# Kernel tuning notes

Hardware: AMD Instinct MI355X
Metric: run time of the kernel (lower is better)

The kernel has to match this reference:

```python
import jax, jax.numpy as jnp
import numpy as np

D_MODEL = 1024
NHEAD = 16
D_K = D_MODEL // NHEAD
NEG_INF = -1e30


def setup_inputs() -> dict:
    key = jax.random.key(0)
    ks = jax.random.split(key, 5)
    seq, batch = 2048, 4
    scale_in = 1.0 / np.sqrt(D_MODEL)
    return {
        "x": jax.random.normal(ks[0], (seq, batch, D_MODEL), dtype=jnp.float32),
        # torch nn.Linear stores weight as (out_features, in_features)
        "w_qkv": jax.random.normal(ks[1], (3 * D_MODEL, D_MODEL), dtype=jnp.float32) * scale_in,
        "b_qkv": jax.random.normal(ks[2], (3 * D_MODEL,), dtype=jnp.float32) * 0.01,
        "w_out": jax.random.normal(ks[3], (D_MODEL, D_MODEL), dtype=jnp.float32) * scale_in,
        "b_out": jax.random.normal(ks[4], (D_MODEL,), dtype=jnp.float32) * 0.01,
        "causal": 1,
    }


def reference(x, w_qkv, b_qkv, w_out, b_out, causal):
    seq, batch, d_model = x.shape
    # fused QKV projection: (seq, batch, 3*d_model)
    qkv = jnp.einsum("sbd,ed->sbe", x, w_qkv) + b_qkv
    q, k, v = jnp.split(qkv, 3, axis=-1)

    def to_heads(t):
        # (seq, batch, d_model) -> (batch*nhead, seq, d_k)
        return t.reshape(seq, batch * NHEAD, D_K).transpose(1, 0, 2)

    q, k, v = to_heads(q), to_heads(k), to_heads(v)
    # full O(seq^2) score tensor, matching the manual implementation
    scores = jnp.einsum("hqd,hkd->hqk", q, k) / (D_K ** 0.5)
    if causal:  # causal is a static Python int, safe under jit as constant
        mask = jnp.triu(jnp.ones((seq, seq), dtype=bool), k=1)
        scores = jnp.where(mask[None, :, :], NEG_INF, scores)
    attn = jax.nn.softmax(scores, axis=-1)
    out = jnp.einsum("hqk,hkd->hqd", attn, v)  # (batch*nhead, seq, d_k)
    out = out.transpose(1, 0, 2).reshape(seq, batch, d_model)
    return jnp.einsum("sbd,ed->sbe", out, w_out) + b_out
```

## Files before the change

### kernel.cpp

```cpp
#include <hip/hip_runtime.h>

typedef __attribute__((ext_vector_type(8))) short short8;
typedef __attribute__((ext_vector_type(4))) float floatx4;
typedef __attribute__((ext_vector_type(16))) float floatx16;
typedef __attribute__((ext_vector_type(4))) unsigned short ushort4v;

__device__ __forceinline__ unsigned short f2bf(float f) {
  unsigned int u = __float_as_uint(f);
  u += 0x7FFFu + ((u >> 16) & 1u);
  return (unsigned short)(u >> 16);
}

__device__ __forceinline__ unsigned int cvt_pk_bf16(float lo, float hi) {
  unsigned int r;
  asm("v_cvt_pk_bf16_f32 %0, %1, %2" : "=v"(r) : "v"(lo), "v"(hi));
  return r;
}

__device__ __forceinline__ void async_copy16(const void* g, void* l) {
  __builtin_amdgcn_global_load_lds(
      (const __attribute__((address_space(1))) unsigned int*)g,
      (__attribute__((address_space(3))) unsigned int*)l, 16, 0, 0);
}

__device__ __forceinline__ float fexp2(float x) {
#if __has_builtin(__builtin_amdgcn_exp2f)
  return __builtin_amdgcn_exp2f(x);
#else
  return exp2f(x);
#endif
}

__global__ __launch_bounds__(256) void cvt_all(const float* __restrict__ x,
                                               const float* __restrict__ wq,
                                               const float* __restrict__ wo,
                                               unsigned short* __restrict__ Xb,
                                               unsigned short* __restrict__ Wqb,
                                               unsigned short* __restrict__ Wob) {
  int i = blockIdx.x * blockDim.x + threadIdx.x;
  const float* src;
  unsigned short* dst;
  int off;
  if (i < 2097152) { src = x;  dst = Xb;  off = i; }
  else if (i < 2883584) { src = wq; dst = Wqb; off = i - 2097152; }
  else { src = wo; dst = Wob; off = i - 2883584; }
  float4 v = reinterpret_cast<const float4*>(src)[off];
  ushort4v o;
  o[0] = f2bf(v.x); o[1] = f2bf(v.y); o[2] = f2bf(v.z); o[3] = f2bf(v.w);
  reinterpret_cast<ushort4v*>(dst)[off] = o;
}

template <int MODE, int NX>
__global__ __launch_bounds__(256, 4) void gemm_nt(const unsigned short* __restrict__ A,
                                                  const unsigned short* __restrict__ B,
                                                  const float* __restrict__ bias,
                                                  void* __restrict__ C,
                                                  int M, int N, int K) {
  __shared__ __align__(16) unsigned short lds[2][128 * 64];
  unsigned short* lA = lds[0];
  unsigned short* lB = lds[1];
  unsigned short* lflat = &lds[0][0];
  const int tid = threadIdx.x;
  const int lane = tid & 63, wave = tid >> 6;
  const int lr = lane & 15, lh = lane >> 4;
  const int chunk = gridDim.x >> 3;
  const int g2 = (blockIdx.x & 7) * chunk + (blockIdx.x >> 3);
  const int m0 = (g2 / NX) * 128, n0 = (g2 % NX) * 128;
  const int wm = (wave >> 1) * 64, wn = (wave & 1) * 64;
  floatx4 acc[4][4] = {};

  for (int k0 = 0; k0 < K; k0 += 64) {
    __syncthreads();
#pragma unroll
    for (int c0 = 0; c0 < 1024; c0 += 256) {
      int L = c0 + tid;
      int r = L >> 3;
      int c = (L & 7) ^ (r & 7);
      async_copy16(A + (size_t)(m0 + r) * K + k0 + c * 8, &lA[(size_t)(c0 + wave * 64) * 8]);
      async_copy16(B + (size_t)(n0 + r) * K + k0 + c * 8, &lB[(size_t)(c0 + wave * 64) * 8]);
    }
    __syncthreads();
#pragma unroll
    for (int kk = 0; kk < 2; ++kk) {
      short8 af[4], bfr[4];
#pragma unroll
      for (int mf = 0; mf < 4; ++mf)
        af[mf] = *(const short8*)&lA[(wm + mf * 16 + lr) * 64 + (((kk * 4 + lh) ^ (lr & 7)) * 8)];
#pragma unroll
      for (int nf = 0; nf < 4; ++nf)
        bfr[nf] = *(const short8*)&lB[(wn + nf * 16 + lr) * 64 + (((kk * 4 + lh) ^ (lr & 7)) * 8)];
#pragma unroll
      for (int mf = 0; mf < 4; ++mf)
#pragma unroll
        for (int nf = 0; nf < 4; ++nf)
          acc[mf][nf] = __builtin_amdgcn_mfma_f32_16x16x32_bf16(af[mf], bfr[nf], acc[mf][nf], 0, 0, 0);
    }
  }

  if (MODE == 1 && (n0 >> 10) == 2) {
    __syncthreads();
#pragma unroll
    for (int mf = 0; mf < 4; ++mf) {
      int sl = (wm >> 2) + mf * 4 + lh;
#pragma unroll
      for (int nf = 0; nf < 4; ++nf) {
        int cl = wn + nf * 16 + lr;
        int hh = cl >> 6, dd = cl & 63;
        int sx = sl ^ ((dd & 3) << 3);
#pragma unroll
        for (int r = 0; r < 4; ++r) {
          float v = acc[mf][nf][r] + bias[n0 + cl];
          lflat[((r * 2 + hh) * 64 + dd) * 32 + sx] = f2bf(v);
        }
      }
    }
    __syncthreads();
    const int hbase = (n0 & 1023) >> 6;
    const int s0g = m0 >> 2;
    unsigned short* V = (unsigned short*)C + (size_t)2 * 64 * 2048 * 64;
#pragma unroll
    for (int k = 0; k < 8; ++k) {
      int f = tid + k * 256;
      int p = f >> 2, q = f & 3;
      int b = p >> 7, hh = (p >> 6) & 1, dd = p & 63;
      int g = b * 16 + hbase + hh;
      int sc = (q ^ (dd & 3)) * 8;
      short8 vv = *(const short8*)&lflat[p * 32 + q * 8];
      *(short8*)&V[((size_t)g * 64 + dd) * 2048 + s0g + sc] = vv;
    }
  } else {
#pragma unroll
    for (int mf = 0; mf < 4; ++mf)
#pragma unroll
      for (int nf = 0; nf < 4; ++nf)
#pragma unroll
        for (int r = 0; r < 4; ++r) {
          int row = m0 + wm + mf * 16 + lh * 4 + r;
          int col = n0 + wn + nf * 16 + lr;
          float v = acc[mf][nf][r] + bias[col];
          if (MODE == 0) {
            ((float*)C)[(size_t)row * N + col] = v;
          } else {
            int part = col >> 10, wi = col & 1023;
            int h = wi >> 6, dd = wi & 63;
            int s = row >> 2, b = row & 3;
            int gg = b * 16 + h;
            size_t base = (size_t)part * (64u * 2048u * 64u);
            if (part == 0) v *= 0.18033688011112042f;
            ((unsigned short*)C)[base + ((size_t)gg * 2048 + s) * 64 + dd] = f2bf(v);
          }
        }
  }
}

__global__ __launch_bounds__(256) void attn_fwd(const unsigned short* __restrict__ Qb,
                                                const unsigned short* __restrict__ Kb,
                                                const unsigned short* __restrict__ Vt,
                                                unsigned short* __restrict__ Att,
                                                const int* __restrict__ causal_p) {
  __shared__ __align__(16) unsigned short smem[16384];
  const int tid = threadIdx.x;
  const int lane = tid & 63, w = tid >> 6;
  const int l31 = lane & 31, hi = lane >> 5;
  const int bid = blockIdx.x;
  const int jj = (bid >> 3) & 3;
  const int mm = (bid >> 5) & 3;
  const int kk2 = (bid >> 8) & 3;
  const int g = (bid & 7) + 8 * ((bid >> 7) & 1) + 16 * mm;
  const int qt = (kk2 == 0) ? (15 - jj) : (kk2 == 1) ? jj : (kk2 == 2) ? (11 - jj) : (4 + jj);
  const int q0 = qt * 128;
  const int causal = causal_p[0];
  const size_t headOff = (size_t)g * 2048 * 64;
  const size_t vtHead = (size_t)g * 64 * 2048;
  const int q0w = q0 + w * 32;
  const int qg = q0w + l31;

  short8 qf[4];
#pragma unroll
  for (int c = 0; c < 4; ++c)
    qf[c] = *(const short8*)&Qb[headOff + (size_t)qg * 64 + c * 16 + hi * 8];

  floatx16 oacc[2] = {};
  float mrow = -1e30f, lrow = 0.f;

  const int nt = causal ? (q0 + 128) / 64 : 2048 / 64;
  const int qmax_w = q0w + 31;

  auto stageK = [&](int buf, int kv0) {
#pragma unroll
    for (int c0 = 0; c0 < 512; c0 += 256) {
      int L = c0 + tid;
      int kvr = L >> 3;
      int c = (tid & 7) ^ (kvr & 7);
      async_copy16(Kb + headOff + (size_t)(kv0 + kvr) * 64 + c * 8,
                   &smem[(size_t)buf * 4096 + (size_t)(c0 + w * 64) * 8]);
    }
  };
  auto stageV = [&](int buf, int kv0) {
#pragma unroll
    for (int c0 = 0; c0 < 512; c0 += 256) {
      int L = c0 + tid;
      int dr = L >> 3;
      int c = (tid & 7) ^ (dr & 7);
      async_copy16(Vt + vtHead + (size_t)dr * 2048 + kv0 + c * 8,
                   &smem[8192 + (size_t)buf * 4096 + (size_t)(c0 + w * 64) * 8]);
    }
  };

  stageK(0, 0);
  stageV(0, 0);
  int cur = 0;

  for (int t = 0; t < nt; ++t) {
    const int kv0 = t * 64;
    if (t + 1 < nt) {
      stageK(cur ^ 1, kv0 + 64);
      stageV(cur ^ 1, kv0 + 64);
      asm volatile("s_waitcnt vmcnt(4)" ::: "memory");
    } else {
      asm volatile("s_waitcnt vmcnt(0)" ::: "memory");
    }
    __builtin_amdgcn_s_barrier();
    asm volatile("" ::: "memory");

    if (!causal || kv0 <= qmax_w) {
      const unsigned short* lK = &smem[(size_t)cur * 4096];
      const unsigned short* lV = &smem[8192 + (size_t)cur * 4096];

      floatx16 sacc[2] = {};
      __builtin_amdgcn_s_setprio(1);
#pragma unroll
      for (int st = 0; st < 2; ++st)
#pragma unroll
        for (int c = 0; c < 4; ++c) {
          int row = st * 32 + l31;
          short8 kf = *(const short8*)&lK[row * 64 + (((2 * c + hi) ^ (row & 7)) * 8)];
          sacc[st] = __builtin_amdgcn_mfma_f32_32x32x16_bf16(kf, qf[c], sacc[st], 0, 0, 0);
        }
      __builtin_amdgcn_s_setprio(0);

      if (causal && kv0 + 63 > q0w) {
#pragma unroll
        for (int st = 0; st < 2; ++st)
#pragma unroll
          for (int r = 0; r < 16; ++r) {
            int kv = kv0 + st * 32 + (r & 3) + 8 * (r >> 2) + 4 * hi;
            if (kv > qg) sacc[st][r] = -1e30f;
          }
      }

      float rm = -1e30f;
#pragma unroll
      for (int st = 0; st < 2; ++st)
#pragma unroll
        for (int r = 0; r < 16; ++r)
          rm = fmaxf(rm, sacc[st][r]);
      rm = fmaxf(rm, __shfl_xor(rm, 32, 64));
      if (!__all(rm - mrow <= 8.f)) {
        float mn = fmaxf(mrow, rm);
        float alpha = fexp2(mrow - mn);
        mrow = mn;
        lrow *= alpha;
#pragma unroll
        for (int dt = 0; dt < 2; ++dt)
#pragma unroll
          for (int r = 0; r < 16; ++r)
            oacc[dt][r] *= alpha;
      }
      float rs = 0.f;
#pragma unroll
      for (int st = 0; st < 2; ++st)
#pragma unroll
        for (int r = 0; r < 16; ++r) {
          float p = fexp2(sacc[st][r] - mrow);
          sacc[st][r] = p;
          rs += p;
        }
      rs += __shfl_xor(rs, 32, 64);
      lrow += rs;

#pragma unroll
      for (int st = 0; st < 2; ++st)
#pragma unroll
        for (int h = 0; h < 2; ++h) {
          unsigned int C1 = cvt_pk_bf16(sacc[st][8 * h + 0], sacc[st][8 * h + 1]);
          unsigned int C2 = cvt_pk_bf16(sacc[st][8 * h + 2], sacc[st][8 * h + 3]);
          unsigned int C3 = cvt_pk_bf16(sacc[st][8 * h + 4], sacc[st][8 * h + 5]);
          unsigned int C4 = cvt_pk_bf16(sacc[st][8 * h + 6], sacc[st][8 * h + 7]);
          unsigned int P1 = hi ? C1 : C3, P2 = hi ? C2 : C4;
          unsigned int R1 = (unsigned int)__shfl_xor((int)P1, 32, 64);
          unsigned int R2 = (unsigned int)__shfl_xor((int)P2, 32, 64);
          union { unsigned int u[4]; short8 s; } pf;
          pf.u[0] = hi ? R1 : C1; pf.u[1] = hi ? R2 : C2;
          pf.u[2] = hi ? C3 : R1; pf.u[3] = hi ? C4 : R2;
          __builtin_amdgcn_s_setprio(1);
#pragma unroll
          for (int dt = 0; dt < 2; ++dt) {
            int row = dt * 32 + l31;
            short8 vf = *(const short8*)&lV[row * 64 + (((st * 4 + h * 2 + hi) ^ (row & 7)) * 8)];
            oacc[dt] = __builtin_amdgcn_mfma_f32_32x32x16_bf16(vf, pf.s, oacc[dt], 0, 0, 0);
          }
          __builtin_amdgcn_s_setprio(0);
        }
    }
    asm volatile("" ::: "memory");
    __builtin_amdgcn_s_barrier();
    cur ^= 1;
  }

  float inv = 1.f / lrow;
#pragma unroll
  for (int dt = 0; dt < 2; ++dt)
#pragma unroll
    for (int r = 0; r < 16; ++r)
      oacc[dt][r] *= inv;

  unsigned short* ov = smem;
  const int ql = w * 32 + l31;
#pragma unroll
  for (int dt = 0; dt < 2; ++dt)
#pragma unroll
    for (int tt = 0; tt < 4; ++tt) {
      int d0 = dt * 32 + 8 * tt + 4 * hi;
      uint2 pk;
      pk.x = cvt_pk_bf16(oacc[dt][4 * tt + 0], oacc[dt][4 * tt + 1]);
      pk.y = cvt_pk_bf16(oacc[dt][4 * tt + 2], oacc[dt][4 * tt + 3]);
      *(uint2*)&ov[ql * 68 + d0] = pk;
    }
  __syncthreads();
  const int bb = g >> 4, hh = g & 15;
#pragma unroll
  for (int k = 0; k < 4; ++k) {
    int row = (tid >> 3) + k * 32;
    short8 vv = *(const short8*)&ov[row * 68 + (tid & 7) * 8];
    int sg = q0 + row;
    *(short8*)&Att[((size_t)sg * 4 + bb) * 1024 + hh * 64 + (tid & 7) * 8] = vv;
  }
}

extern "C" void kernel_launch(void* const* d_in, const int* in_sizes, int n_in,
                              void* d_out, int out_size, void* d_ws, size_t ws_size,
                              hipStream_t stream) {
  const float* x     = (const float*)d_in[0];
  const float* w_qkv = (const float*)d_in[1];
  const float* b_qkv = (const float*)d_in[2];
  const float* w_out = (const float*)d_in[3];
  const float* b_out = (const float*)d_in[4];
  const int*   causal = (const int*)d_in[5];
  float* out = (float*)d_out;

  char* ws = (char*)d_ws;
  size_t off = 0;
  auto alloc = [&](size_t bytes) { char* p = ws + off; off += (bytes + 255) & ~(size_t)255; return p; };
  unsigned short* Xbf  = (unsigned short*)alloc((size_t)8192 * 1024 * 2);
  unsigned short* Wqkv = (unsigned short*)alloc((size_t)3072 * 1024 * 2);
  unsigned short* Wout = (unsigned short*)alloc((size_t)1024 * 1024 * 2);
  unsigned short* QKV  = (unsigned short*)alloc((size_t)3 * 64 * 2048 * 64 * 2);
  unsigned short* Att  = (unsigned short*)alloc((size_t)8192 * 1024 * 2);
  (void)ws_size; (void)in_sizes; (void)n_in; (void)out_size;

  cvt_all<<<12288, 256, 0, stream>>>(x, w_qkv, w_out, Xbf, Wqkv, Wout);

  gemm_nt<1, 24><<<24 * 64, 256, 0, stream>>>(Xbf, Wqkv, b_qkv, (void*)QKV, 8192, 3072, 1024);

  const unsigned short* Qh = QKV;
  const unsigned short* Kh = QKV + (size_t)64 * 2048 * 64;
  const unsigned short* Vh = QKV + (size_t)2 * 64 * 2048 * 64;
  attn_fwd<<<1024, 256, 0, stream>>>(Qh, Kh, Vh, Att, causal);

  gemm_nt<0, 8><<<8 * 64, 256, 0, stream>>>(Att, Wout, b_out, (void*)out, 8192, 1024, 1024);
}
```

Measured before the change: 154.3 us.

## Split attention KV range across two wave groups and merge softmax partials

The attention kernel now launches 512 threads per block. Two groups of four waves each process half of the KV tiles for the same 128-query tile, each with its own double-buffered LDS region. The partial max, sum and output of the second group go through shared memory, and the first group merges them flash-decoding style before writing out. This adds intra-block parallelism on the KV dimension to cut per-block latency, at the cost of doubled LDS (64KB), fewer resident blocks and an extra merge and sync pass.

```diff
diff --git a/kernel.cpp b/kernel.cpp
--- a/kernel.cpp
+++ b/kernel.cpp
@@ -153,26 +153,27 @@
   }
 }
 
-__global__ __launch_bounds__(256) void attn_fwd(const unsigned short* __restrict__ Qb,
+__global__ __launch_bounds__(512) void attn_fwd(const unsigned short* __restrict__ Qb,
                                                 const unsigned short* __restrict__ Kb,
                                                 const unsigned short* __restrict__ Vt,
                                                 unsigned short* __restrict__ Att,
                                                 const int* __restrict__ causal_p) {
-  __shared__ __align__(16) unsigned short smem[16384];
+  __shared__ __align__(16) unsigned short smem[32768];
   const int tid = threadIdx.x;
   const int lane = tid & 63, w = tid >> 6;
+  const int w4 = w & 3, ch = w >> 2;
+  const int t256 = tid & 255;
   const int l31 = lane & 31, hi = lane >> 5;
   const int bid = blockIdx.x;
   const int jj = (bid >> 3) & 3;
-  const int mm = (bid >> 5) & 3;
-  const int kk2 = (bid >> 8) & 3;
-  const int g = (bid & 7) + 8 * ((bid >> 7) & 1) + 16 * mm;
-  const int qt = (kk2 == 0) ? (15 - jj) : (kk2 == 1) ? jj : (kk2 == 2) ? (11 - jj) : (4 + jj);
+  const int u = (bid >> 8) & 1, v = (bid >> 9) & 1;
+  const int g = (bid & 7) + 8 * ((bid >> 7) & 1) + 16 * ((bid >> 5) & 3);
+  const int qt = (v == 0) ? (u ? (11 - jj) : (15 - jj)) : (u ? (4 + jj) : jj);
   const int q0 = qt * 128;
   const int causal = causal_p[0];
   const size_t headOff = (size_t)g * 2048 * 64;
   const size_t vtHead = (size_t)g * 64 * 2048;
-  const int q0w = q0 + w * 32;
+  const int q0w = q0 + w4 * 32;
   const int qg = q0w + l31;
 
   short8 qf[4];
@@ -183,37 +184,39 @@
   floatx16 oacc[2] = {};
   float mrow = -1e30f, lrow = 0.f;
 
-  const int nt = causal ? (q0 + 128) / 64 : 2048 / 64;
+  const int nt = causal ? (2 * qt + 2) : 32;
+  const int half = nt >> 1;
+  const int tbase = ch * half;
   const int qmax_w = q0w + 31;
 
   auto stageK = [&](int buf, int kv0) {
 #pragma unroll
     for (int c0 = 0; c0 < 512; c0 += 256) {
-      int L = c0 + tid;
+      int L = c0 + t256;
       int kvr = L >> 3;
-      int c = (tid & 7) ^ (kvr & 7);
+      int c = (t256 & 7) ^ (kvr & 7);
       async_copy16(Kb + headOff + (size_t)(kv0 + kvr) * 64 + c * 8,
-                   &smem[(size_t)buf * 4096 + (size_t)(c0 + w * 64) * 8]);
+                   &smem[(size_t)ch * 8192 + (size_t)buf * 4096 + (size_t)(c0 + w4 * 64) * 8]);
     }
   };
   auto stageV = [&](int buf, int kv0) {
 #pragma unroll
     for (int c0 = 0; c0 < 512; c0 += 256) {
-      int L = c0 + tid;
+      int L = c0 + t256;
       int dr = L >> 3;
-      int c = (tid & 7) ^ (dr & 7);
+      int c = (t256 & 7) ^ (dr & 7);
       async_copy16(Vt + vtHead + (size_t)dr * 2048 + kv0 + c * 8,
-                   &smem[8192 + (size_t)buf * 4096 + (size_t)(c0 + w * 64) * 8]);
+                   &smem[16384 + (size_t)ch * 8192 + (size_t)buf * 4096 + (size_t)(c0 + w4 * 64) * 8]);
     }
   };
 
-  stageK(0, 0);
-  stageV(0, 0);
+  stageK(0, tbase * 64);
+  stageV(0, tbase * 64);
   int cur = 0;
 
-  for (int t = 0; t < nt; ++t) {
-    const int kv0 = t * 64;
-    if (t + 1 < nt) {
+  for (int tl = 0; tl < half; ++tl) {
+    const int kv0 = (tbase + tl) * 64;
+    if (tl + 1 < half) {
       stageK(cur ^ 1, kv0 + 64);
       stageV(cur ^ 1, kv0 + 64);
       asm volatile("s_waitcnt vmcnt(4)" ::: "memory");
@@ -224,8 +227,8 @@
     asm volatile("" ::: "memory");
 
     if (!causal || kv0 <= qmax_w) {
-      const unsigned short* lK = &smem[(size_t)cur * 4096];
-      const unsigned short* lV = &smem[8192 + (size_t)cur * 4096];
+      const unsigned short* lK = &smem[(size_t)ch * 8192 + (size_t)cur * 4096];
+      const unsigned short* lV = &smem[16384 + (size_t)ch * 8192 + (size_t)cur * 4096];
 
       floatx16 sacc[2] = {};
       __builtin_amdgcn_s_setprio(1);
@@ -290,9 +293,9 @@
           unsigned int P1 = hi ? C1 : C3, P2 = hi ? C2 : C4;
           unsigned int R1 = (unsigned int)__shfl_xor((int)P1, 32, 64);
           unsigned int R2 = (unsigned int)__shfl_xor((int)P2, 32, 64);
-          union { unsigned int u[4]; short8 s; } pf;
-          pf.u[0] = hi ? R1 : C1; pf.u[1] = hi ? R2 : C2;
-          pf.u[2] = hi ? C3 : R1; pf.u[3] = hi ? C4 : R2;
+          union { unsigned int u4[4]; short8 s; } pf;
+          pf.u4[0] = hi ? R1 : C1; pf.u4[1] = hi ? R2 : C2;
+          pf.u4[2] = hi ? C3 : R1; pf.u4[3] = hi ? C4 : R2;
           __builtin_amdgcn_s_setprio(1);
 #pragma unroll
           for (int dt = 0; dt < 2; ++dt) {
@@ -308,33 +311,57 @@
     cur ^= 1;
   }
 
-  float inv = 1.f / lrow;
-#pragma unroll
-  for (int dt = 0; dt < 2; ++dt)
-#pragma unroll
-    for (int r = 0; r < 16; ++r)
-      oacc[dt][r] *= inv;
-
-  unsigned short* ov = smem;
-  const int ql = w * 32 + l31;
-#pragma unroll
-  for (int dt = 0; dt < 2; ++dt)
-#pragma unroll
-    for (int tt = 0; tt < 4; ++tt) {
-      int d0 = dt * 32 + 8 * tt + 4 * hi;
-      uint2 pk;
-      pk.x = cvt_pk_bf16(oacc[dt][4 * tt + 0], oacc[dt][4 * tt + 1]);
-      pk.y = cvt_pk_bf16(oacc[dt][4 * tt + 2], oacc[dt][4 * tt + 3]);
-      *(uint2*)&ov[ql * 68 + d0] = pk;
-    }
+  float* mg = (float*)smem;
+  if (ch == 1) {
+    if (hi == 0) {
+      mg[w4 * 2112 + l31] = mrow;
+      mg[w4 * 2112 + 32 + l31] = lrow;
+    }
+#pragma unroll
+    for (int dt = 0; dt < 2; ++dt)
+#pragma unroll
+      for (int r = 0; r < 16; ++r) {
+        int d = dt * 32 + (r & 3) + 8 * (r >> 2) + 4 * hi;
+        mg[w4 * 2112 + 64 + l31 * 64 + d] = oacc[dt][r];
+      }
+  }
   __syncthreads();
+
+  unsigned short* ov = &smem[18432];
+  if (ch == 0) {
+    float m2 = mg[w4 * 2112 + l31];
+    float l2 = mg[w4 * 2112 + 32 + l31];
+    float m12 = fmaxf(mrow, m2);
+    float a1 = fexp2(mrow - m12);
+    float a2 = fexp2(m2 - m12);
+    float inv = 1.f / (lrow * a1 + l2 * a2);
+    const int ql = w4 * 32 + l31;
+#pragma unroll
+    for (int dt = 0; dt < 2; ++dt)
+#pragma unroll
+      for (int tt = 0; tt < 4; ++tt) {
+        int d0 = dt * 32 + 8 * tt + 4 * hi;
+        float om[4];
+#pragma unroll
+        for (int i = 0; i < 4; ++i)
+          om[i] = (oacc[dt][4 * tt + i] * a1 +
+                   mg[w4 * 2112 + 64 + l31 * 64 + d0 + i] * a2) * inv;
+        uint2 pk;
+        pk.x = cvt_pk_bf16(om[0], om[1]);
+        pk.y = cvt_pk_bf16(om[2], om[3]);
+        *(uint2*)&ov[ql * 68 + d0] = pk;
+      }
+  }
+  __syncthreads();
+
   const int bb = g >> 4, hh = g & 15;
 #pragma unroll
-  for (int k = 0; k < 4; ++k) {
-    int row = (tid >> 3) + k * 32;
-    short8 vv = *(const short8*)&ov[row * 68 + (tid & 7) * 8];
+  for (int k = 0; k < 2; ++k) {
+    int idx = tid + k * 512;
+    int row = idx >> 3;
+    short8 vv = *(const short8*)&ov[row * 68 + (idx & 7) * 8];
     int sg = q0 + row;
-    *(short8*)&Att[((size_t)sg * 4 + bb) * 1024 + hh * 64 + (tid & 7) * 8] = vv;
+    *(short8*)&Att[((size_t)sg * 4 + bb) * 1024 + hh * 64 + (idx & 7) * 8] = vv;
   }
 }
 
@@ -366,7 +393,7 @@
   const unsigned short* Qh = QKV;
   const unsigned short* Kh = QKV + (size_t)64 * 2048 * 64;
   const unsigned short* Vh = QKV + (size_t)2 * 64 * 2048 * 64;
-  attn_fwd<<<1024, 256, 0, stream>>>(Qh, Kh, Vh, Att, causal);
+  attn_fwd<<<1024, 512, 0, stream>>>(Qh, Kh, Vh, Att, causal);
 
   gemm_nt<0, 8><<<8 * 64, 256, 0, stream>>>(Att, Wout, b_out, (void*)out, 8192, 1024, 1024);
 }
```

Result: slower. 158.1 us (+2.5%).
